# Optimization experiments

Hardware: AMD Instinct MI355X
Metric: run time of the kernel (lower is better)

The kernel has to match this reference:

```python
import jax, jax.numpy as jnp
import numpy as np

B = 16384       # batch of peptide samples
M = 15          # max_peptide_size
R = 64          # aa_rep_size
P = 34          # number of pocket positions
F = 9           # filter_size
A = 20          # alphabet size


def setup_inputs() -> dict:
    key = jax.random.key(0)
    k1, k2, k3, k4 = jax.random.split(key, 4)
    peptide_encoding = jax.random.normal(k1, (B, M, R), dtype=jnp.float32)
    pocket_aa_idx = jax.random.randint(k2, (B, P), 0, A, dtype=jnp.int32)
    adj_mask = jax.random.randint(k3, (B, P, M), 0, 2, dtype=jnp.int32)
    # one trainable 1-D filter of length F per alphabet letter ('uniform' init)
    kernels = jax.random.uniform(k4, (A, F), dtype=jnp.float32, minval=-0.05, maxval=0.05)
    return {"peptide_encoding": peptide_encoding, "pocket_aa_idx": pocket_aa_idx,
            "adj_mask": adj_mask, "kernels": kernels}


def reference(peptide_encoding, pocket_aa_idx, adj_mask, kernels):
    # Per pocket position p of sample b: filter = kernels[pocket_aa_idx[b,p]]  [B,P,F]
    filt = kernels[pocket_aa_idx]
    # Convolution is linear, so sum the adjacent peptide-position encodings first:
    # s[b,p,r] = sum_m adj_mask[b,p,m] * peptide_encoding[b,m,r]   -> [B,P,R]
    s = jnp.einsum('bpm,bmr->bpr', adj_mask.astype(peptide_encoding.dtype), peptide_encoding)
    # Full convolution along the representation axis: output length R + F - 1
    conv1 = jax.vmap(jax.vmap(lambda a, b: jnp.convolve(a, b, mode='full')))
    out = conv1(s, filt)  # [B, P, R+F-1]
    return out
```

## Files before the change

### kernel.cpp

```cpp
#include <hip/hip_runtime.h>

#define MM 15
#define RR 64
#define PP 34
#define FF 9
#define AA 20
#define OW 72
#define AJ 16

#define WAVE_SHL1 0x130
#define WAVE_SHR1 0x138

__device__ __forceinline__ float dpp_shr1(float x) {
    return __int_as_float(__builtin_amdgcn_update_dpp(
        0, __float_as_int(x), WAVE_SHR1, 0xF, 0xF, true));
}
__device__ __forceinline__ float dpp_shl1(float x) {
    return __int_as_float(__builtin_amdgcn_update_dpp(
        0, __float_as_int(x), WAVE_SHL1, 0xF, 0xF, true));
}

__global__ __launch_bounds__(256)
void ppc_kernel(const float* __restrict__ pe,
                const int*   __restrict__ idx,
                const int*   __restrict__ adj,
                const float* __restrict__ kernels,
                float*       __restrict__ out)
{
    const int b    = blockIdx.x;
    const int t    = threadIdx.x;
    const int lane = t & 63;
    const int w    = t >> 6;

    __shared__ float s_adjf[PP * AJ];

    const float* peb  = pe  + (size_t)b * (MM * RR);
    const int*   adjb = adj + (size_t)b * (PP * MM);
    const int*   idxb = idx + (size_t)b * PP;
    float*       outb = out + (size_t)b * (PP * OW);

    #pragma unroll
    for (int k = 0; k < 2; ++k) {
        const int i = t + k * 256;
        if (i < PP * MM) {
            const int p = (unsigned)i / MM, m = i - p * MM;
            s_adjf[p * AJ + m] = (float)adjb[i];
        }
    }
    if (t < PP) s_adjf[t * AJ + 15] = 0.0f;

    float pv[MM];
    #pragma unroll
    for (int m = 0; m < MM; ++m) pv[m] = peb[m * RR + lane];

    __syncthreads();

    #pragma unroll
    for (int j = 0; j < 9; ++j) {
        const int p = w + 4 * j;
        if (p < PP) {
            const float* g = &s_adjf[p * AJ];
            const float4 g0 = *(const float4*)&g[0];
            const float4 g1 = *(const float4*)&g[4];
            const float4 g2 = *(const float4*)&g[8];
            const float4 g3 = *(const float4*)&g[12];
            float a0, a1, a2;
            a0 = g0.x * pv[0];  a1 = g0.y * pv[1];  a2 = g0.z * pv[2];
            a0 = fmaf(g0.w, pv[3],  a0);
            a1 = fmaf(g1.x, pv[4],  a1);
            a2 = fmaf(g1.y, pv[5],  a2);
            a0 = fmaf(g1.z, pv[6],  a0);
            a1 = fmaf(g1.w, pv[7],  a1);
            a2 = fmaf(g2.x, pv[8],  a2);
            a0 = fmaf(g2.y, pv[9],  a0);
            a1 = fmaf(g2.z, pv[10], a1);
            a2 = fmaf(g2.w, pv[11], a2);
            a0 = fmaf(g3.x, pv[12], a0);
            a1 = fmaf(g3.y, pv[13], a1);
            a2 = fmaf(g3.z, pv[14], a2);
            const float s = (a0 + a1) + a2;

            const float* kb = kernels + idxb[p] * FF;
            float kf[FF];
            #pragma unroll
            for (int i2 = 0; i2 < FF; ++i2) kf[i2] = kb[i2];

            float H = kf[8] * s;
            #pragma unroll
            for (int i2 = 7; i2 >= 0; --i2)
                H = fmaf(kf[i2], s, dpp_shr1(H));
            outb[p * OW + lane] = H;

            float T = kf[0] * s;
            #pragma unroll
            for (int i2 = 1; i2 <= 8; ++i2)
                T = fmaf(kf[i2], s, dpp_shl1(T));
            if (lane >= 56)
                outb[p * OW + 8 + lane] = T;
        }
    }
}

extern "C" void kernel_launch(void* const* d_in, const int* in_sizes, int n_in,
                              void* d_out, int out_size, void* d_ws, size_t ws_size,
                              hipStream_t stream) {
    const float* pe      = (const float*)d_in[0];
    const int*   idx     = (const int*)  d_in[1];
    const int*   adj     = (const int*)  d_in[2];
    const float* kernels = (const float*)d_in[3];
    float*       out     = (float*)d_out;

    const int B = in_sizes[0] / (MM * RR);
    ppc_kernel<<<B, 256, 0, stream>>>(pe, idx, adj, kernels, out);
}
```

Before: 85.49 us.

## Batch adjacency sums across pockets and compute conv tail via shared memory

Loads all nine pockets' adjacency rows into registers and computes their reductions with independent accumulators, exposing more ILP. Pocket indices are staged in shared memory. The second DPP chain for the tail outputs is replaced by writing the last eight sums to shared memory, where 8-lane groups compute the tail elements directly. This removes half the DPP shifts and the partial-wave tail stores, but adds register pressure and relies on an LDS waitcnt rather than a barrier, which is only safe because each wave reads just its own slot.

```diff
diff --git a/kernel.cpp b/kernel.cpp
--- a/kernel.cpp
+++ b/kernel.cpp
@@ -8,16 +8,10 @@
 #define OW 72
 #define AJ 16
 
-#define WAVE_SHL1 0x130
 #define WAVE_SHR1 0x138
-
 __device__ __forceinline__ float dpp_shr1(float x) {
     return __int_as_float(__builtin_amdgcn_update_dpp(
         0, __float_as_int(x), WAVE_SHR1, 0xF, 0xF, true));
-}
-__device__ __forceinline__ float dpp_shl1(float x) {
-    return __int_as_float(__builtin_amdgcn_update_dpp(
-        0, __float_as_int(x), WAVE_SHL1, 0xF, 0xF, true));
 }
 
 __global__ __launch_bounds__(256)
@@ -33,11 +27,16 @@
     const int w    = t >> 6;
 
     __shared__ float s_adjf[PP * AJ];
+    __shared__ int   s_idx[PP];
+    __shared__ float s_tail[4][9][8];
 
     const float* peb  = pe  + (size_t)b * (MM * RR);
     const int*   adjb = adj + (size_t)b * (PP * MM);
-    const int*   idxb = idx + (size_t)b * PP;
     float*       outb = out + (size_t)b * (PP * OW);
+
+    float pv[MM];
+    #pragma unroll
+    for (int m = 0; m < MM; ++m) pv[m] = peb[m * RR + lane];
 
     #pragma unroll
     for (int k = 0; k < 2; ++k) {
@@ -47,56 +46,95 @@
             s_adjf[p * AJ + m] = (float)adjb[i];
         }
     }
-    if (t < PP) s_adjf[t * AJ + 15] = 0.0f;
+    if (t < PP) {
+        s_adjf[t * AJ + 15] = 0.0f;
+        s_idx[t] = idx[(size_t)b * PP + t];
+    }
+    __syncthreads();
 
-    float pv[MM];
+    float4 G[9][4];
     #pragma unroll
-    for (int m = 0; m < MM; ++m) pv[m] = peb[m * RR + lane];
+    for (int j = 0; j < 9; ++j) {
+        const int p = w + 4 * j;
+        if (p < PP) {
+            const float* g = &s_adjf[p * AJ];
+            G[j][0] = *(const float4*)&g[0];
+            G[j][1] = *(const float4*)&g[4];
+            G[j][2] = *(const float4*)&g[8];
+            G[j][3] = *(const float4*)&g[12];
+        } else {
+            G[j][0] = G[j][1] = G[j][2] = G[j][3] = make_float4(0.f,0.f,0.f,0.f);
+        }
+    }
 
-    __syncthreads();
+    float acc[9] = {0.f,0.f,0.f,0.f,0.f,0.f,0.f,0.f,0.f};
+    #pragma unroll
+    for (int mc = 0; mc < 4; ++mc) {
+        #pragma unroll
+        for (int mm = 0; mm < 4; ++mm) {
+            const int m = mc * 4 + mm;
+            if (m < MM) {
+                #pragma unroll
+                for (int j = 0; j < 9; ++j) {
+                    const float gv = (&G[j][mc].x)[mm];
+                    acc[j] = fmaf(gv, pv[m], acc[j]);
+                }
+            }
+        }
+    }
 
     #pragma unroll
     for (int j = 0; j < 9; ++j) {
         const int p = w + 4 * j;
         if (p < PP) {
-            const float* g = &s_adjf[p * AJ];
-            const float4 g0 = *(const float4*)&g[0];
-            const float4 g1 = *(const float4*)&g[4];
-            const float4 g2 = *(const float4*)&g[8];
-            const float4 g3 = *(const float4*)&g[12];
-            float a0, a1, a2;
-            a0 = g0.x * pv[0];  a1 = g0.y * pv[1];  a2 = g0.z * pv[2];
-            a0 = fmaf(g0.w, pv[3],  a0);
-            a1 = fmaf(g1.x, pv[4],  a1);
-            a2 = fmaf(g1.y, pv[5],  a2);
-            a0 = fmaf(g1.z, pv[6],  a0);
-            a1 = fmaf(g1.w, pv[7],  a1);
-            a2 = fmaf(g2.x, pv[8],  a2);
-            a0 = fmaf(g2.y, pv[9],  a0);
-            a1 = fmaf(g2.z, pv[10], a1);
-            a2 = fmaf(g2.w, pv[11], a2);
-            a0 = fmaf(g3.x, pv[12], a0);
-            a1 = fmaf(g3.y, pv[13], a1);
-            a2 = fmaf(g3.z, pv[14], a2);
-            const float s = (a0 + a1) + a2;
-
-            const float* kb = kernels + idxb[p] * FF;
+            const int a = s_idx[p];
+            const float* kb = kernels + a * FF;
             float kf[FF];
             #pragma unroll
-            for (int i2 = 0; i2 < FF; ++i2) kf[i2] = kb[i2];
+            for (int i = 0; i < FF; ++i) kf[i] = kb[i];
 
+            const float s = acc[j];
             float H = kf[8] * s;
             #pragma unroll
-            for (int i2 = 7; i2 >= 0; --i2)
-                H = fmaf(kf[i2], s, dpp_shr1(H));
+            for (int i = 7; i >= 0; --i)
+                H = fmaf(kf[i], s, dpp_shr1(H));
             outb[p * OW + lane] = H;
 
-            float T = kf[0] * s;
+            if (lane >= 56) s_tail[w][j][lane - 56] = s;
+        }
+    }
+
+    asm volatile("s_waitcnt lgkmcnt(0)" ::: "memory");
+
+    {
+        const int jj = lane >> 3;
+        const int u  = lane & 7;
+        const int p  = w + 4 * jj;
+        const float* sv = &s_tail[w][jj][0];
+        const float* kb = kernels + s_idx[p] * FF;
+        float acc2 = 0.f;
+        #pragma unroll
+        for (int i = 1; i <= 8; ++i) {
+            const float kv = kb[i];
+            const float svv = sv[(8 + u - i) & 7];
+            acc2 += (i > u) ? kv * svv : 0.f;
+        }
+        outb[p * OW + 64 + u] = acc2;
+    }
+    {
+        const int p = w + 32;
+        if (p < PP && lane < 8) {
+            const int u = lane;
+            const float* sv = &s_tail[w][8][0];
+            const float* kb = kernels + s_idx[p] * FF;
+            float acc2 = 0.f;
             #pragma unroll
-            for (int i2 = 1; i2 <= 8; ++i2)
-                T = fmaf(kf[i2], s, dpp_shl1(T));
-            if (lane >= 56)
-                outb[p * OW + 8 + lane] = T;
+            for (int i = 1; i <= 8; ++i) {
+                const float kv = kb[i];
+                const float svv = sv[(8 + u - i) & 7];
+                acc2 += (i > u) ? kv * svv : 0.f;
+            }
+            outb[p * OW + 64 + u] = acc2;
         }
     }
 }
```

Result: slower. 165.3 us (+93.3%).
